# Kernel optimization log

Measured on AMD Instinct MI355X. Metric: run time of the kernel, lower is better.

The kernel has to match this reference:

```python
import jax, jax.numpy as jnp
import numpy as np

_EPS = 1e-6

def _qmul(q1, q2):  # xyzw quaternion product
    x1, y1, z1, w1 = q1[..., 0], q1[..., 1], q1[..., 2], q1[..., 3]
    x2, y2, z2, w2 = q2[..., 0], q2[..., 1], q2[..., 2], q2[..., 3]
    return jnp.stack([
        w1 * x2 + x1 * w2 + y1 * z2 - z1 * y2,
        w1 * y2 + y1 * w2 + z1 * x2 - x1 * z2,
        w1 * z2 + z1 * w2 + x1 * y2 - y1 * x2,
        w1 * w2 - x1 * x2 - y1 * y2 - z1 * z2], axis=-1)

def _qrot(q, v):  # rotate v by unit quaternion q (xyzw)
    qv, qw = q[..., :3], q[..., 3:4]
    t = 2.0 * jnp.cross(qv, v)
    return v + qw * t + jnp.cross(qv, t)

def _so3_log(q):  # quaternion (xyzw) -> rotation vector phi
    qv, qw = q[..., :3], q[..., 3:4]
    n2 = jnp.sum(qv * qv, axis=-1, keepdims=True)
    small = n2 < _EPS * _EPS
    n = jnp.sqrt(jnp.where(small, 1.0, n2))
    factor = jnp.where(small,
                       2.0 / qw - (2.0 / 3.0) * n2 / qw ** 3,
                       2.0 * jnp.arctan2(n, qw) / n)
    return factor * qv

def _so3_exp(phi):  # rotation vector -> quaternion (xyzw)
    t2 = jnp.sum(phi * phi, axis=-1, keepdims=True)
    small = t2 < _EPS * _EPS
    theta = jnp.sqrt(jnp.where(small, 1.0, t2))
    half = 0.5 * theta
    s = jnp.where(small, 0.5 - t2 / 48.0, jnp.sin(half) / theta)
    w = jnp.where(small, 1.0 - t2 / 8.0, jnp.cos(half))
    return jnp.concatenate([s * phi, w], axis=-1)

def _jl(phi, v):  # SO3 left Jacobian J_l(phi) @ v
    t2 = jnp.sum(phi * phi, axis=-1, keepdims=True)
    small = t2 < _EPS * _EPS
    t2s = jnp.where(small, 1.0, t2)
    theta = jnp.sqrt(t2s)
    a = jnp.where(small, 0.5 - t2 / 24.0, (1.0 - jnp.cos(theta)) / t2s)
    b = jnp.where(small, 1.0 / 6.0 - t2 / 120.0, (theta - jnp.sin(theta)) / (t2s * theta))
    c1 = jnp.cross(phi, v)
    return v + a * c1 + b * jnp.cross(phi, c1)

def _jl_inv(phi, v):  # SO3 left Jacobian inverse J_l^{-1}(phi) @ v
    t2 = jnp.sum(phi * phi, axis=-1, keepdims=True)
    small = t2 < _EPS * _EPS
    t2s = jnp.where(small, 1.0, t2)
    theta = jnp.sqrt(t2s)
    s = jnp.sin(theta)
    s_safe = jnp.where(jnp.abs(s) < _EPS, _EPS, s)
    c = jnp.where(small, 1.0 / 12.0 + t2 / 720.0,
                  1.0 / t2s - (1.0 + jnp.cos(theta)) / (2.0 * theta * s_safe))
    c1 = jnp.cross(phi, v)
    return v - 0.5 * c1 + c * jnp.cross(phi, c1)

def _se3_inv(T):
    t, q = T[..., :3], T[..., 3:]
    qi = q * jnp.array([-1.0, -1.0, -1.0, 1.0], dtype=T.dtype)
    return jnp.concatenate([-_qrot(qi, t), qi], axis=-1)

def _se3_mul(T1, T2):
    t1, q1 = T1[..., :3], T1[..., 3:]
    t2, q2 = T2[..., :3], T2[..., 3:]
    return jnp.concatenate([t1 + _qrot(q1, t2), _qmul(q1, q2)], axis=-1)

def _se3_log(T):  # SE3 -> se3 [tau, phi]
    t, q = T[..., :3], T[..., 3:]
    phi = _so3_log(q)
    return jnp.concatenate([_jl_inv(phi, t), phi], axis=-1)

def _se3_exp(xi):  # se3 [tau, phi] -> SE3
    tau, phi = xi[..., :3], xi[..., 3:]
    q = _so3_exp(phi)
    return jnp.concatenate([_jl(phi, tau), q], axis=-1)

def _forward(input_poses, time):
    # duplicate first/last pose (inter_begin_and_end=True)
    poses = jnp.concatenate([input_poses[:, :1], input_poses, input_poses[:, -1:]], axis=1)
    B, P = poses.shape[0], poses.shape[1]
    S = P - 3  # number of spline segments
    u = time.reshape(-1)  # [K]
    K = u.shape[0]
    U = jnp.stack([jnp.ones_like(u), u, u * u, u * u * u], axis=0)  # [4,K]
    M = jnp.array([[5., 3., -3., 1.], [1., 3., 3., -2.], [0., 0., 0., 1.]], dtype=u.dtype) / 6.0
    w = M @ U  # [3,K] cumulative B-spline weights
    p0, p1 = poses[:, 0:S], poses[:, 1:S + 1]
    p2, p3 = poses[:, 2:S + 2], poses[:, 3:S + 3]
    d0 = _se3_log(_se3_mul(_se3_inv(p0), p1))  # [B,S,6]
    d1 = _se3_log(_se3_mul(_se3_inv(p1), p2))
    d2 = _se3_log(_se3_mul(_se3_inv(p2), p3))
    A0 = _se3_exp(d0[:, :, None, :] * w[0][None, None, :, None])  # [B,S,K,7]
    A1 = _se3_exp(d1[:, :, None, :] * w[1][None, None, :, None])
    A2 = _se3_exp(d2[:, :, None, :] * w[2][None, None, :, None])
    Td = jnp.broadcast_to(p0[:, :, None, :], (B, S, K, 7))
    out = _se3_mul(_se3_mul(_se3_mul(Td, A0), A1), A2)
    return out.reshape(B, S * K, 7)

def setup_inputs() -> dict:
    key = jax.random.key(0)
    k1, k2, k3 = jax.random.split(key, 3)
    B, N, K = 32, 2048, 32
    t = jax.random.normal(k1, (B, N, 3), dtype=jnp.float32) * 2.0
    q = jax.random.normal(k2, (B, N, 4), dtype=jnp.float32)
    q = q / jnp.linalg.norm(q, axis=-1, keepdims=True)
    q = jnp.where(q[..., 3:4] < 0, -q, q)  # qw >= 0 for well-conditioned Log
    input_poses = jnp.concatenate([t, q], axis=-1)
    time = jax.random.uniform(k3, (1, 1, K), dtype=jnp.float32)
    return {"input_poses": input_poses, "time": time}

def reference(input_poses, time):
    return _forward(input_poses, time)
```

## Files before the change

### kernel.cpp

```cpp
#include <hip/hip_runtime.h>
#include <cmath>

namespace {

constexpr int BATCH  = 32;
constexpr int NPOSE  = 2048;
constexpr int KSAMP  = 32;
constexpr int NSEG   = NPOSE - 1;
constexpr int NDELTA = NPOSE + 1;
constexpr int SEGB   = 32;
constexpr float EPS  = 1e-6f;
constexpr float EPS2 = 1e-12f;
constexpr float INV_TWO_PI = 0.15915494309189535f;

struct V3 { float x, y, z; };
struct Q4 { float x, y, z, w; };
struct SE3 { V3 t; Q4 q; };

__device__ __forceinline__ float frcp(float x)  { return __builtin_amdgcn_rcpf(x); }
__device__ __forceinline__ float fsqrt(float x) { return __builtin_amdgcn_sqrtf(x); }
__device__ __forceinline__ float fsin(float x)  { return __builtin_amdgcn_sinf(x * INV_TWO_PI); }
__device__ __forceinline__ float fcos(float x)  { return __builtin_amdgcn_cosf(x * INV_TWO_PI); }

__device__ __forceinline__ V3 v3add(V3 a, V3 b) { return {a.x + b.x, a.y + b.y, a.z + b.z}; }
__device__ __forceinline__ V3 v3sub(V3 a, V3 b) { return {a.x - b.x, a.y - b.y, a.z - b.z}; }
__device__ __forceinline__ V3 v3scl(V3 a, float s) { return {a.x * s, a.y * s, a.z * s}; }
__device__ __forceinline__ float v3dot(V3 a, V3 b) { return a.x * b.x + a.y * b.y + a.z * b.z; }
__device__ __forceinline__ V3 v3cross(V3 a, V3 b) {
    return {a.y * b.z - a.z * b.y, a.z * b.x - a.x * b.z, a.x * b.y - a.y * b.x};
}

__device__ __forceinline__ V3 qrot(Q4 q, V3 v) {
    V3 qv{q.x, q.y, q.z};
    V3 t = v3scl(v3cross(qv, v), 2.0f);
    return v3add(v3add(v, v3scl(t, q.w)), v3cross(qv, t));
}

__device__ __forceinline__ Q4 qmul(Q4 a, Q4 b) {
    return {a.w * b.x + a.x * b.w + a.y * b.z - a.z * b.y,
            a.w * b.y + a.y * b.w + a.z * b.x - a.x * b.z,
            a.w * b.z + a.z * b.w + a.x * b.y - a.y * b.x,
            a.w * b.w - a.x * b.x - a.y * b.y - a.z * b.z};
}

__device__ __forceinline__ SE3 se3_mul(SE3 A, SE3 Bv) {
    SE3 r;
    r.t = v3add(A.t, qrot(A.q, Bv.t));
    r.q = qmul(A.q, Bv.q);
    return r;
}

__device__ __forceinline__ float facos(float x) {
    float ax = fabsf(x);
    float p = -0.0012624911f;
    p = p * ax + 0.0066700901f;
    p = p * ax - 0.0170881256f;
    p = p * ax + 0.0308918810f;
    p = p * ax - 0.0501743046f;
    p = p * ax + 0.0889789874f;
    p = p * ax - 0.2145988016f;
    p = p * ax + 1.5707963050f;
    float r = fsqrt(fmaxf(1.0f - ax, 0.0f)) * p;
    return (x >= 0.0f) ? r : (3.14159265358979f - r);
}

__device__ __forceinline__ V3 so3_log(Q4 q) {
    V3 qv{q.x, q.y, q.z};
    float n2 = v3dot(qv, qv);
    bool small = n2 < EPS2;
    float n = fsqrt(small ? 1.0f : n2);
    float iw = frcp(q.w);
    float f_small = 2.0f * iw - (2.0f / 3.0f) * n2 * iw * iw * iw;
    float wc = fminf(fmaxf(q.w, -1.0f), 1.0f);
    float f_big = 2.0f * facos(wc) * frcp(n);
    return v3scl(qv, small ? f_small : f_big);
}

__device__ __forceinline__ V3 jl_inv(V3 phi, V3 v) {
    float t2 = v3dot(phi, phi);
    bool small = t2 < EPS2;
    float t2s = small ? 1.0f : t2;
    float theta = fsqrt(t2s);
    float s = fsin(theta), cth = fcos(theta);
    float s_safe = (fabsf(s) < EPS) ? EPS : s;
    float c_big = frcp(t2s) - (1.0f + cth) * frcp(2.0f * theta * s_safe);
    float c = small ? (1.0f / 12.0f + t2 * (1.0f / 720.0f)) : c_big;
    V3 c1 = v3cross(phi, v);
    return v3add(v3sub(v, v3scl(c1, 0.5f)), v3scl(v3cross(phi, c1), c));
}

__global__ __launch_bounds__(256) void lie_delta_kernel(
    const float* __restrict__ poses,
    float4* __restrict__ ws)
{
    const int i = blockIdx.x * 256 + threadIdx.x;
    const int b = blockIdx.y;
    if (i >= NDELTA) return;

    int ia = max(i - 1, 0);
    int ib = min(i, NPOSE - 1);
    const float* Pa = poses + ((size_t)b * NPOSE + ia) * 7;
    const float* Pb = poses + ((size_t)b * NPOSE + ib) * 7;
    V3 ta{Pa[0], Pa[1], Pa[2]}; Q4 qa{Pa[3], Pa[4], Pa[5], Pa[6]};
    V3 tb{Pb[0], Pb[1], Pb[2]}; Q4 qb{Pb[3], Pb[4], Pb[5], Pb[6]};

    Q4 qi{-qa.x, -qa.y, -qa.z, qa.w};
    V3 trel = qrot(qi, v3sub(tb, ta));
    Q4 qrel = qmul(qi, qb);
    V3 phi = so3_log(qrel);
    V3 tau = jl_inv(phi, trel);

    float n2 = v3dot(phi, phi);
    float nphi = fsqrt(n2);
    float inv_n = frcp(fmaxf(nphi, 1e-20f));
    V3 u  = v3scl(phi, inv_n);
    V3 c1 = v3cross(u, tau);
    V3 c2 = v3cross(u, c1);

    float4* row = ws + ((size_t)b * NDELTA + i) * 4;
    row[0] = make_float4(tau.x, tau.y, tau.z, nphi);
    row[1] = make_float4(u.x,  u.y,  u.z,  0.0f);
    row[2] = make_float4(c1.x, c1.y, c1.z, 0.0f);
    row[3] = make_float4(c2.x, c2.y, c2.z, 0.0f);
}

__device__ __forceinline__ SE3 exp_fast(float4 A, float4 U, float4 C1, float4 C2, float w) {
    float th = fmaxf(w * A.w, 1e-12f);
    float sh = fsin(0.5f * th), ch = fcos(0.5f * th);
    float it = frcp(th);
    float sA = 2.0f * sh * sh * it;
    float sB = 1.0f - 2.0f * sh * ch * it;
    SE3 r;
    r.q = {sh * U.x, sh * U.y, sh * U.z, ch};
    r.t = {w * (A.x + sA * C1.x + sB * C2.x),
           w * (A.y + sA * C1.y + sB * C2.y),
           w * (A.z + sA * C1.z + sB * C2.z)};
    return r;
}

__global__ __launch_bounds__(256) void lie_spline_kernel(
    const float* __restrict__ poses,
    const float* __restrict__ timev,
    const float4* __restrict__ ws,
    float* __restrict__ out)
{
    __shared__ float4 sdel[(SEGB + 2) * 5];
    __shared__ float  sp[SEGB * 8];
    __shared__ float  sw[3 * KSAMP];

    const int b   = blockIdx.y;
    const int s0  = blockIdx.x * SEGB;
    const int tid = threadIdx.x;

    if (tid < (SEGB + 2) * 4) {
        int row = tid >> 2, r = tid & 3;
        int idx = min(s0 + row, NDELTA - 1);
        sdel[row * 5 + r] = ws[((size_t)b * NDELTA + idx) * 4 + r];
    }
    if (tid < SEGB * 7) {
        int jseg = tid / 7, c = tid - jseg * 7;
        int ip = min(max(s0 + jseg - 1, 0), NPOSE - 1);
        sp[jseg * 8 + c] = poses[((size_t)b * NPOSE + ip) * 7 + c];
    }
    if (tid >= 224) {
        int l = tid - 224;
        float u = timev[l];
        float u2 = u * u, u3 = u2 * u;
        const float c6 = 1.0f / 6.0f;
        sw[l]             = (5.0f + 3.0f * u - 3.0f * u2 + u3) * c6;
        sw[KSAMP + l]     = (1.0f + 3.0f * u + 3.0f * u2 - 2.0f * u3) * c6;
        sw[2 * KSAMP + l] = u3 * c6;
    }
    __syncthreads();

    const int segl = tid >> 3;
    const int s    = s0 + segl;
    if (s >= NSEG) return;
    const int k0   = (tid & 7) * 4;

    const float4* R0 = sdel + segl * 5;
    const float4* R1 = R0 + 5;
    const float4* R2 = R0 + 10;
    float4 A0 = R0[0], U0 = R0[1], C10 = R0[2], C20 = R0[3];
    float4 A1 = R1[0], U1 = R1[1], C11 = R1[2], C21 = R1[3];
    float4 A2 = R2[0], U2 = R2[1], C12 = R2[2], C22 = R2[3];

    const float* P0 = sp + segl * 8;
    const SE3 Tp{{P0[0], P0[1], P0[2]}, {P0[3], P0[4], P0[5], P0[6]}};

    float buf[4 * 7];
    #pragma unroll
    for (int j = 0; j < 4; ++j) {
        int k = k0 + j;
        float w0 = sw[k], w1 = sw[KSAMP + k], w2 = sw[2 * KSAMP + k];
        SE3 T = se3_mul(Tp, exp_fast(A0, U0, C10, C20, w0));
        T = se3_mul(T, exp_fast(A1, U1, C11, C21, w1));
        T = se3_mul(T, exp_fast(A2, U2, C12, C22, w2));
        float* d = buf + j * 7;
        d[0] = T.t.x; d[1] = T.t.y; d[2] = T.t.z;
        d[3] = T.q.x; d[4] = T.q.y; d[5] = T.q.z; d[6] = T.q.w;
    }

    float4* ov = reinterpret_cast<float4*>(
        out + ((size_t)b * NSEG + s0) * (size_t)(KSAMP * 7) + (size_t)tid * 28);
    #pragma unroll
    for (int c = 0; c < 7; ++c)
        ov[c] = make_float4(buf[4 * c], buf[4 * c + 1], buf[4 * c + 2], buf[4 * c + 3]);
}

}

extern "C" void kernel_launch(void* const* d_in, const int* in_sizes, int n_in,
                              void* d_out, int out_size, void* d_ws, size_t ws_size,
                              hipStream_t stream) {
    const float* poses = (const float*)d_in[0];
    const float* timev = (const float*)d_in[1];
    float* out = (float*)d_out;
    float4* ws = (float4*)d_ws;
    (void)in_sizes; (void)n_in; (void)out_size; (void)ws_size;

    dim3 g1((NDELTA + 255) / 256, BATCH);
    lie_delta_kernel<<<g1, 256, 0, stream>>>(poses, ws);

    dim3 g2((NSEG + SEGB - 1) / SEGB, BATCH);
    lie_spline_kernel<<<g2, 256, 0, stream>>>(poses, timev, ws, out);
}
```

Measured before the change: 95.44 us.

## Stage spline outputs through LDS for coalesced stores and compute weights inline

Each thread now writes its 28 output floats into a shared-memory staging buffer, and after a barrier the whole block copies that buffer to global memory as contiguous float4s with a strided loop. Previously each thread stored 7 float4s at a 112-byte stride, leaving neighbouring lanes' writes interleaved. The shared arrays for pose and spline weights are removed: each thread loads its anchor pose straight from global memory and computes the B-spline weights in registers from one float4 of time values. The cost is a 28 KB LDS buffer, which may reduce occupancy, plus an extra barrier and a round trip through LDS.

```diff
diff --git a/kernel.cpp b/kernel.cpp
--- a/kernel.cpp
+++ b/kernel.cpp
@@ -145,8 +145,7 @@
     float* __restrict__ out)
 {
     __shared__ float4 sdel[(SEGB + 2) * 5];
-    __shared__ float  sp[SEGB * 8];
-    __shared__ float  sw[3 * KSAMP];
+    __shared__ __align__(16) float stage[SEGB * KSAMP * 7];
 
     const int b   = blockIdx.y;
     const int s0  = blockIdx.x * SEGB;
@@ -157,42 +156,33 @@
         int idx = min(s0 + row, NDELTA - 1);
         sdel[row * 5 + r] = ws[((size_t)b * NDELTA + idx) * 4 + r];
     }
-    if (tid < SEGB * 7) {
-        int jseg = tid / 7, c = tid - jseg * 7;
-        int ip = min(max(s0 + jseg - 1, 0), NPOSE - 1);
-        sp[jseg * 8 + c] = poses[((size_t)b * NPOSE + ip) * 7 + c];
-    }
-    if (tid >= 224) {
-        int l = tid - 224;
-        float u = timev[l];
+
+    const int segl = tid >> 3;
+    const int s    = s0 + segl;
+    const int m    = tid & 7;
+
+    int ip = min(max(s - 1, 0), NPOSE - 1);
+    const float* P0 = poses + ((size_t)b * NPOSE + ip) * 7;
+    const SE3 Tp{{P0[0], P0[1], P0[2]}, {P0[3], P0[4], P0[5], P0[6]}};
+    float4 uvec = reinterpret_cast<const float4*>(timev)[m];
+
+    __syncthreads();
+
+    const float4* R = sdel + segl * 5;
+    float4 A0 = R[0],  U0 = R[1],  C10 = R[2],  C20 = R[3];
+    float4 A1 = R[5],  U1 = R[6],  C11 = R[7],  C21 = R[8];
+    float4 A2 = R[10], U2 = R[11], C12 = R[12], C22 = R[13];
+
+    __align__(16) float buf[28];
+    const float us[4] = {uvec.x, uvec.y, uvec.z, uvec.w};
+    #pragma unroll
+    for (int j = 0; j < 4; ++j) {
+        float u  = us[j];
         float u2 = u * u, u3 = u2 * u;
         const float c6 = 1.0f / 6.0f;
-        sw[l]             = (5.0f + 3.0f * u - 3.0f * u2 + u3) * c6;
-        sw[KSAMP + l]     = (1.0f + 3.0f * u + 3.0f * u2 - 2.0f * u3) * c6;
-        sw[2 * KSAMP + l] = u3 * c6;
-    }
-    __syncthreads();
-
-    const int segl = tid >> 3;
-    const int s    = s0 + segl;
-    if (s >= NSEG) return;
-    const int k0   = (tid & 7) * 4;
-
-    const float4* R0 = sdel + segl * 5;
-    const float4* R1 = R0 + 5;
-    const float4* R2 = R0 + 10;
-    float4 A0 = R0[0], U0 = R0[1], C10 = R0[2], C20 = R0[3];
-    float4 A1 = R1[0], U1 = R1[1], C11 = R1[2], C21 = R1[3];
-    float4 A2 = R2[0], U2 = R2[1], C12 = R2[2], C22 = R2[3];
-
-    const float* P0 = sp + segl * 8;
-    const SE3 Tp{{P0[0], P0[1], P0[2]}, {P0[3], P0[4], P0[5], P0[6]}};
-
-    float buf[4 * 7];
-    #pragma unroll
-    for (int j = 0; j < 4; ++j) {
-        int k = k0 + j;
-        float w0 = sw[k], w1 = sw[KSAMP + k], w2 = sw[2 * KSAMP + k];
+        float w0 = (5.0f + 3.0f * u - 3.0f * u2 + u3) * c6;
+        float w1 = (1.0f + 3.0f * u + 3.0f * u2 - 2.0f * u3) * c6;
+        float w2 = u3 * c6;
         SE3 T = se3_mul(Tp, exp_fast(A0, U0, C10, C20, w0));
         T = se3_mul(T, exp_fast(A1, U1, C11, C21, w1));
         T = se3_mul(T, exp_fast(A2, U2, C12, C22, w2));
@@ -201,11 +191,19 @@
         d[3] = T.q.x; d[4] = T.q.y; d[5] = T.q.z; d[6] = T.q.w;
     }
 
-    float4* ov = reinterpret_cast<float4*>(
-        out + ((size_t)b * NSEG + s0) * (size_t)(KSAMP * 7) + (size_t)tid * 28);
-    #pragma unroll
-    for (int c = 0; c < 7; ++c)
-        ov[c] = make_float4(buf[4 * c], buf[4 * c + 1], buf[4 * c + 2], buf[4 * c + 3]);
+    if (s < NSEG) {
+        float4* sv = reinterpret_cast<float4*>(stage + segl * (KSAMP * 7) + m * 28);
+        const float4* bv = reinterpret_cast<const float4*>(buf);
+        #pragma unroll
+        for (int c = 0; c < 7; ++c) sv[c] = bv[c];
+    }
+    __syncthreads();
+
+    int nseg_blk = min(NSEG - s0, SEGB);
+    int nvec = nseg_blk * (KSAMP * 7 / 4);
+    const float4* svv = reinterpret_cast<const float4*>(stage);
+    float4* ov = reinterpret_cast<float4*>(out + ((size_t)b * NSEG + s0) * (size_t)(KSAMP * 7));
+    for (int j = tid; j < nvec; j += 256) ov[j] = svv[j];
 }
 
 }
```

Measured after the change: 90.02 us. 5.7% less time.
